# Kernel optimization log

Measured on AMD Instinct MI355X. Metric: run time of the kernel, lower is better.

## Reference

```python
import jax, jax.numpy as jnp
import numpy as np

B_SZ = 2
SEQ = 2048
D_MODEL = 2048
D_INNER = 4096
D_STATE = 128
D_CONV = 4
HEADDIM = 64
NHEADS = D_INNER // HEADDIM
CHUNK = 256
EPS = 1e-5


def segsum(a):
    # a: (..., T) -> (..., T, T) lower-triangular segment sums, -inf above diag
    T = a.shape[-1]
    cs = jnp.cumsum(a, axis=-1)
    ss = cs[..., :, None] - cs[..., None, :]
    mask = jnp.tril(jnp.ones((T, T), dtype=bool))
    return jnp.where(mask, ss, -jnp.inf)


def setup_inputs() -> dict:
    key = jax.random.key(0)
    ks = jax.random.split(key, 8)
    conv_dim = D_INNER + 2 * D_STATE
    d_in_proj = 2 * D_INNER + 2 * D_STATE + NHEADS
    x = jax.random.normal(ks[0], (B_SZ, SEQ, D_MODEL), jnp.float32)
    in_proj_w = jax.random.normal(ks[1], (d_in_proj, D_MODEL), jnp.float32) * 0.02
    conv_w = jax.random.normal(ks[2], (conv_dim, D_CONV), jnp.float32) * 0.2
    conv_b = jnp.zeros((conv_dim,), jnp.float32)
    dt0 = jax.random.uniform(ks[3], (NHEADS,), jnp.float32, 0.001, 0.1)
    dt_bias = jnp.log(jnp.expm1(dt0))  # inverse-softplus init as in mamba_ssm
    A_log = jnp.log(jax.random.uniform(ks[4], (NHEADS,), jnp.float32, 1.0, 16.0))
    D = jnp.ones((NHEADS,), jnp.float32)
    norm_w = jnp.ones((D_INNER,), jnp.float32)
    out_proj_w = jax.random.normal(ks[5], (D_MODEL, D_INNER), jnp.float32) * 0.02
    return {"x": x, "in_proj_w": in_proj_w, "conv_w": conv_w, "conv_b": conv_b,
            "dt_bias": dt_bias, "A_log": A_log, "D": D, "norm_w": norm_w,
            "out_proj_w": out_proj_w}


def reference(x, in_proj_w, conv_w, conv_b, dt_bias, A_log, D, norm_w, out_proj_w):
    b, L, _ = x.shape
    conv_dim = D_INNER + 2 * D_STATE
    # in_proj -> [z, xBC, dt]
    zxbcdt = jnp.einsum('bld,ed->ble', x, in_proj_w)
    z = zxbcdt[..., :D_INNER]
    xBC = zxbcdt[..., D_INNER:D_INNER + conv_dim]
    dt = jax.nn.softplus(zxbcdt[..., D_INNER + conv_dim:] + dt_bias)  # (b,L,H)
    # causal depthwise conv1d + silu
    xBC_t = jnp.transpose(xBC, (0, 2, 1))  # (b, conv_dim, L)
    conv_out = jax.lax.conv_general_dilated(
        xBC_t, conv_w[:, None, :], window_strides=(1,),
        padding=[(D_CONV - 1, 0)], feature_group_count=conv_dim)
    xBC = jax.nn.silu(jnp.transpose(conv_out + conv_b[:, None], (0, 2, 1)))
    x_ssm = xBC[..., :D_INNER].reshape(b, L, NHEADS, HEADDIM)
    Bm = xBC[..., D_INNER:D_INNER + D_STATE]          # (b,L,N) ngroups=1
    Cm = xBC[..., D_INNER + D_STATE:]                  # (b,L,N)
    A = -jnp.exp(A_log)                                # (H,)
    dA = dt * A                                        # (b,L,H)
    X = x_ssm * dt[..., None]                          # (b,L,H,P)
    # chunked SSD
    nc = L // CHUNK
    Xc = X.reshape(b, nc, CHUNK, NHEADS, HEADDIM)
    dAc = jnp.transpose(dA.reshape(b, nc, CHUNK, NHEADS), (0, 3, 1, 2))  # (b,h,c,l)
    Bc = Bm.reshape(b, nc, CHUNK, D_STATE)
    Cc = Cm.reshape(b, nc, CHUNK, D_STATE)
    Lmat = jnp.exp(segsum(dAc))                        # (b,h,c,l,l)
    Y_diag = jnp.einsum('bcln,bcsn,bhcls,bcshp->bclhp', Cc, Bc, Lmat, Xc)
    A_cs = jnp.cumsum(dAc, axis=-1)                    # (b,h,c,l)
    decay_states = jnp.exp(A_cs[..., -1:] - A_cs)
    states = jnp.einsum('bcln,bhcl,bclhp->bchpn', Bc, decay_states, Xc)
    chunk_sum = jnp.pad(A_cs[..., -1], ((0, 0), (0, 0), (1, 0)))  # (b,h,c+1)
    decay_chunk = jnp.exp(segsum(chunk_sum))           # (b,h,c+1,c+1)
    states_cat = jnp.concatenate([jnp.zeros_like(states[:, :1]), states], axis=1)
    prev = jnp.einsum('bhzc,bchpn->bzhpn', decay_chunk, states_cat)[:, :-1]
    Y_off = jnp.einsum('bcln,bchpn,bhcl->bclhp', Cc, prev, jnp.exp(A_cs))
    Y = (Y_diag + Y_off).reshape(b, L, NHEADS, HEADDIM)
    Y = Y + x_ssm * D[:, None]                          # skip connection per head
    y = Y.reshape(b, L, D_INNER)
    # gated RMSNorm: norm(y * silu(z)) * weight
    yg = y * jax.nn.silu(z)
    var = jnp.mean(yg * yg, axis=-1, keepdims=True)
    y = yg * jax.lax.rsqrt(var + EPS) * norm_w
    return jnp.einsum('ble,de->bld', y, out_proj_w)
```

## Files before the change

kernel.cpp:

```cpp
#include <hip/hip_runtime.h>
#include <math.h>

#define NBSZ 2
#define SEQ 2048
#define DMODEL 2048
#define DINNER 4096
#define DSTATE 128
#define NHEADS 64
#define CHUNK 256
#define NC 8
#define CONVDIM 4352
#define DINPROJ 8512

typedef unsigned short ushort_t;
typedef short short8 __attribute__((ext_vector_type(8)));
typedef float f32x4 __attribute__((ext_vector_type(4)));

__device__ __forceinline__ float bf2f(ushort_t u){
  union { float f; unsigned u; } x; x.u = ((unsigned)u) << 16; return x.f;
}
__device__ __forceinline__ ushort_t f2bf(float f){
  union { float f; unsigned u; } x; x.f = f;
  unsigned u = x.u;
  unsigned r = (u + 0x7fffu + ((u >> 16) & 1u)) >> 16;
  return (ushort_t)r;
}
__device__ __forceinline__ float exp_neg(float a){
  return expf(fminf(a, 0.f));
}
__device__ __forceinline__ void gload_lds16(const void* g, void* l) {
  __builtin_amdgcn_global_load_lds(
      (const __attribute__((address_space(1))) unsigned int*)g,
      (__attribute__((address_space(3))) unsigned int*)l, 16, 0, 0);
}

#define N_X   8388608LL
#define O_WIN 8388608LL
#define O_CW  25821184LL
#define O_CB  25838592LL
#define O_DTB 25842944LL
#define O_AL  25843008LL
#define O_DD  25843072LL
#define O_NW  25843136LL
#define O_WO  25847232LL
#define N_TOT 34235840LL
#define N_GRP (N_TOT / 8)

__global__ __launch_bounds__(256)
void convert_inputs(const void* __restrict__ x, const void* __restrict__ w_in,
                    const void* __restrict__ cw, const void* __restrict__ cb,
                    const void* __restrict__ dtb, const void* __restrict__ alog,
                    const void* __restrict__ dd, const void* __restrict__ nw,
                    const void* __restrict__ wout, ushort_t* __restrict__ dst) {
  bool bf = (((const unsigned*)dd)[0] == 0x3F803F80u);
  long long stride = (long long)gridDim.x * 256LL;
  for (long long g = (long long)blockIdx.x * 256 + threadIdx.x; g < N_GRP; g += stride) {
    long long i = g * 8;
    const void* src; long long off;
    if      (i < O_WIN) { src = x;    off = i; }
    else if (i < O_CW)  { src = w_in; off = i - O_WIN; }
    else if (i < O_CB)  { src = cw;   off = i - O_CW; }
    else if (i < O_DTB) { src = cb;   off = i - O_CB; }
    else if (i < O_AL)  { src = dtb;  off = i - O_DTB; }
    else if (i < O_DD)  { src = alog; off = i - O_AL; }
    else if (i < O_NW)  { src = dd;   off = i - O_DD; }
    else if (i < O_WO)  { src = nw;   off = i - O_NW; }
    else                { src = wout; off = i - O_WO; }
    if (bf) {
      *(int4*)(dst + i) = *(const int4*)((const ushort_t*)src + off);
    } else {
      float4 a = *(const float4*)((const float*)src + off);
      float4 b = *(const float4*)((const float*)src + off + 4);
      short8 o;
      o[0] = (short)f2bf(a.x); o[1] = (short)f2bf(a.y);
      o[2] = (short)f2bf(a.z); o[3] = (short)f2bf(a.w);
      o[4] = (short)f2bf(b.x); o[5] = (short)f2bf(b.y);
      o[6] = (short)f2bf(b.z); o[7] = (short)f2bf(b.w);
      *(short8*)(dst + i) = o;
    }
  }
}

__global__ __launch_bounds__(256)
void gemm_bt(const ushort_t* __restrict__ A, const ushort_t* __restrict__ B,
             ushort_t* __restrict__ C, int M, int N, int K) {
  __shared__ __align__(16) ushort_t sA[128][64];
  __shared__ __align__(16) ushort_t sB[128][64];
  int tid = threadIdx.x;
  int wave = tid >> 6, lane = tid & 63, quad = lane >> 4, l16 = lane & 15;
  int m0 = blockIdx.x * 128, n0 = blockIdx.y * 128;
  int wm = (wave >> 1) * 64, wn = (wave & 1) * 64;
  int rsub = lane >> 3, csub = lane & 7;
  int swc = ((csub ^ rsub) & 7) * 8;
  int srow = wave * 8 + rsub;
  f32x4 acc[4][4] = {};
  int r7 = l16 & 7;
  for (int k0 = 0; k0 < K; k0 += 64) {
    const ushort_t* Ag = A + (size_t)(m0 + srow) * K + k0 + swc;
#pragma unroll
    for (int i = 0; i < 4; ++i)
      gload_lds16(Ag + (size_t)(i * 32) * K, &sA[wave * 8 + i * 32][0]);
#pragma unroll
    for (int i = 0; i < 4; ++i) {
      int br = n0 + srow + i * 32;
      if (br > N - 1) br = N - 1;
      gload_lds16(B + (size_t)br * K + k0 + swc, &sB[wave * 8 + i * 32][0]);
    }
    __syncthreads();
#pragma unroll
    for (int kk = 0; kk < 64; kk += 32) {
      int g = (kk >> 3) + quad;
      int sw = ((g ^ r7) & 7) * 8;
      short8 af[4], bfr[4];
#pragma unroll
      for (int i = 0; i < 4; ++i) af[i]  = *(const short8*)&sA[wm + i*16 + l16][sw];
#pragma unroll
      for (int j = 0; j < 4; ++j) bfr[j] = *(const short8*)&sB[wn + j*16 + l16][sw];
#pragma unroll
      for (int i = 0; i < 4; ++i)
#pragma unroll
        for (int j = 0; j < 4; ++j)
          acc[i][j] = __builtin_amdgcn_mfma_f32_16x16x32_bf16(af[i], bfr[j], acc[i][j], 0, 0, 0);
    }
    __syncthreads();
  }
#pragma unroll
  for (int i = 0; i < 4; ++i) {
    int row = m0 + wm + i*16 + quad*4;
#pragma unroll
    for (int j = 0; j < 4; ++j) {
      int col = n0 + wn + j*16 + l16;
      if (col < N) {
#pragma unroll
        for (int r = 0; r < 4; ++r)
          C[(size_t)(row + r) * N + col] = f2bf(acc[i][j][r]);
      }
    }
  }
}

__global__ __launch_bounds__(256)
void gemm_bt_splitk(const ushort_t* __restrict__ A, const ushort_t* __restrict__ B,
                    ushort_t* __restrict__ Cpart, int M, int N, int Kstride, int Klen) {
  __shared__ __align__(16) ushort_t sA[128][64];
  __shared__ __align__(16) ushort_t sB[128][64];
  int tid = threadIdx.x;
  int wave = tid >> 6, lane = tid & 63, quad = lane >> 4, l16 = lane & 15;
  int m0 = blockIdx.x * 128, n0 = blockIdx.y * 128;
  int wm = (wave >> 1) * 64, wn = (wave & 1) * 64;
  int rsub = lane >> 3, csub = lane & 7;
  int swc = ((csub ^ rsub) & 7) * 8;
  int srow = wave * 8 + rsub;
  const ushort_t* Ab = A + (size_t)blockIdx.z * Klen;
  const ushort_t* Bb = B + (size_t)blockIdx.z * Klen;
  ushort_t* Cp = Cpart + (size_t)blockIdx.z * M * N;
  f32x4 acc[4][4] = {};
  int r7 = l16 & 7;
  for (int k0 = 0; k0 < Klen; k0 += 64) {
    const ushort_t* Ag = Ab + (size_t)(m0 + srow) * Kstride + k0 + swc;
    const ushort_t* Bg = Bb + (size_t)(n0 + srow) * Kstride + k0 + swc;
#pragma unroll
    for (int i = 0; i < 4; ++i)
      gload_lds16(Ag + (size_t)(i * 32) * Kstride, &sA[wave * 8 + i * 32][0]);
#pragma unroll
    for (int i = 0; i < 4; ++i)
      gload_lds16(Bg + (size_t)(i * 32) * Kstride, &sB[wave * 8 + i * 32][0]);
    __syncthreads();
#pragma unroll
    for (int kk = 0; kk < 64; kk += 32) {
      int g = (kk >> 3) + quad;
      int sw = ((g ^ r7) & 7) * 8;
      short8 af[4], bfr[4];
#pragma unroll
      for (int i = 0; i < 4; ++i) af[i]  = *(const short8*)&sA[wm + i*16 + l16][sw];
#pragma unroll
      for (int j = 0; j < 4; ++j) bfr[j] = *(const short8*)&sB[wn + j*16 + l16][sw];
#pragma unroll
      for (int i = 0; i < 4; ++i)
#pragma unroll
        for (int j = 0; j < 4; ++j)
          acc[i][j] = __builtin_amdgcn_mfma_f32_16x16x32_bf16(af[i], bfr[j], acc[i][j], 0, 0, 0);
    }
    __syncthreads();
  }
#pragma unroll
  for (int i = 0; i < 4; ++i) {
    int row = m0 + wm + i*16 + quad*4;
#pragma unroll
    for (int j = 0; j < 4; ++j) {
      int col = n0 + wn + j*16 + l16;
#pragma unroll
      for (int r = 0; r < 4; ++r)
        Cp[(size_t)(row + r) * N + col] = f2bf(acc[i][j][r]);
    }
  }
}

__global__ __launch_bounds__(256)
void reduce_out(const ushort_t* __restrict__ p0, const ushort_t* __restrict__ p1,
                void* __restrict__ out, const unsigned* __restrict__ probe) {
  long long i = ((long long)blockIdx.x * 256 + threadIdx.x) * 8;
  short8 a = *(const short8*)(p0 + i);
  short8 b = *(const short8*)(p1 + i);
  float v[8];
#pragma unroll
  for (int q = 0; q < 8; ++q) {
    v[q] = bf2f((ushort_t)a[q]) + bf2f((ushort_t)b[q]);
    if (!(fabsf(v[q]) < 1e30f)) v[q] = 12345.0f;
  }
  if (probe[0] == 0x3F800000u) {
    float* of = (float*)out + i;
    *(float4*)of     = {v[0], v[1], v[2], v[3]};
    *(float4*)(of+4) = {v[4], v[5], v[6], v[7]};
  } else {
    short8 s;
#pragma unroll
    for (int q = 0; q < 8; ++q) s[q] = (short)f2bf(v[q]);
    *(short8*)((ushort_t*)out + i) = s;
  }
}

__global__ __launch_bounds__(256)
void conv_silu(const ushort_t* __restrict__ zx, const ushort_t* __restrict__ cw,
               const ushort_t* __restrict__ cb, ushort_t* __restrict__ xbc) {
  int idx = blockIdx.x * 256 + threadIdx.x;
  int c8 = (idx % (CONVDIM / 8)) * 8;
  int l  = (idx / (CONVDIM / 8)) % SEQ;
  int b  = idx / ((CONVDIM / 8) * SEQ);
  float acc[8];
  short8 bias = *(const short8*)(cb + c8);
#pragma unroll
  for (int q = 0; q < 8; ++q) acc[q] = bf2f((ushort_t)bias[q]);
  short8 wv[4];
#pragma unroll
  for (int m = 0; m < 4; ++m) wv[m] = *(const short8*)(cw + c8 * 4 + m * 8);
#pragma unroll
  for (int k = 0; k < 4; ++k) {
    int ll = l - 3 + k;
    if (ll >= 0) {
      short8 xv = *(const short8*)(zx + ((size_t)b * SEQ + ll) * DINPROJ + DINNER + c8);
#pragma unroll
      for (int q = 0; q < 8; ++q) {
        int j = q * 4 + k;
        acc[q] += bf2f((ushort_t)xv[q]) * bf2f((ushort_t)wv[j >> 3][j & 7]);
      }
    }
  }
  short8 o;
#pragma unroll
  for (int q = 0; q < 8; ++q) {
    float sig = 1.f / (1.f + expf(-acc[q]));
    o[q] = (short)f2bf(acc[q] * sig);
  }
  *(short8*)(xbc + ((size_t)b * SEQ + l) * CONVDIM + c8) = o;
}

__global__ __launch_bounds__(256)
void transpose_B(const ushort_t* __restrict__ xbc, ushort_t* __restrict__ Bt) {
  __shared__ ushort_t tile[64][72];
  int bid = blockIdx.x;
  int ft = bid & 1;
  int st = (bid >> 1) & 31;
  int b  = bid >> 6;
  int t = threadIdx.x;
  int r = t >> 2, c0 = (t & 3) * 16;
  const ushort_t* src = xbc + ((size_t)b * SEQ + st * 64 + r) * CONVDIM + DINNER + ft * 64 + c0;
  *(int4*)&tile[r][c0]     = *(const int4*)src;
  *(int4*)&tile[r][c0 + 8] = *(const int4*)(src + 8);
  __syncthreads();
  int f = t >> 2, s0 = (t & 3) * 16;
  ushort_t tmp[16];
#pragma unroll
  for (int q = 0; q < 16; ++q) tmp[q] = tile[s0 + q][f];
  ushort_t* dst = Bt + ((size_t)b * 128 + ft * 64 + f) * SEQ + st * 64 + s0;
  *(int4*)dst       = *(int4*)&tmp[0];
  *(int4*)(dst + 8) = *(int4*)&tmp[8];
}

__global__ __launch_bounds__(256)
void chunk_cumsum(const ushort_t* __restrict__ zx, const ushort_t* __restrict__ dt_bias,
                  const ushort_t* __restrict__ A_log,
                  float* __restrict__ dt, float* __restrict__ cs) {
  int bid = blockIdx.x;
  int c = bid % NC, h = (bid / NC) % NHEADS, b = bid / (NC * NHEADS);
  int t = threadIdx.x;
  int l = c * CHUNK + t;
  float v = bf2f(zx[(size_t)(b * SEQ + l) * DINPROJ + DINNER + CONVDIM + h]) + bf2f(dt_bias[h]);
  float sp = (v > 20.f) ? v : log1pf(expf(v));
  dt[(size_t)(b * SEQ + l) * NHEADS + h] = sp;
  float A = -expf(bf2f(A_log[h]));
  __shared__ float sh[CHUNK];
  sh[t] = sp * A; __syncthreads();
  for (int off = 1; off < CHUNK; off <<= 1) {
    float add = (t >= off) ? sh[t - off] : 0.f;
    __syncthreads();
    sh[t] += add;
    __syncthreads();
  }
  cs[(size_t)bid * CHUNK + t] = sh[t];
}

__global__ __launch_bounds__(256)
void states_kernel(const ushort_t* __restrict__ xbc, const ushort_t* __restrict__ Bt,
                   const float* __restrict__ dt, const float* __restrict__ cs,
                   float* __restrict__ states) {
  int bid = blockIdx.x;
  int h = bid % NHEADS, c = (bid / NHEADS) % NC, b = bid / (NHEADS * NC);
  int tid = threadIdx.x, wave = tid >> 6, lane = tid & 63, quad = lane >> 4, l16 = lane & 15;
  __shared__ __align__(16) ushort_t sXt[64][264];
  int l0 = c * CHUNK;
  const float* csC = cs + ((size_t)((b * NHEADS + h) * NC + c)) * CHUNK;
  {
    int l = tid;
    float cl = csC[CHUNK - 1];
    float scale = dt[((size_t)b * SEQ + l0 + l) * NHEADS + h] * exp_neg(cl - csC[l]);
    const ushort_t* xrow = xbc + ((size_t)b * SEQ + l0 + l) * CONVDIM + h * 64;
#pragma unroll
    for (int pp = 0; pp < 64; pp += 8) {
      short8 v = *(const short8*)(xrow + pp);
#pragma unroll
      for (int q = 0; q < 8; ++q) sXt[pp + q][l] = f2bf(bf2f((ushort_t)v[q]) * scale);
    }
  }
  __syncthreads();
  f32x4 acc[4][2] = {};
  for (int ks = 0; ks < 8; ++ks) {
    int k0 = ks * 32;
    short8 bfr[2];
#pragma unroll
    for (int j = 0; j < 2; ++j) {
      int n = wave * 32 + j * 16 + l16;
      bfr[j] = *(const short8*)(Bt + ((size_t)b * 128 + n) * SEQ + l0 + k0 + quad * 8);
    }
#pragma unroll
    for (int i = 0; i < 4; ++i) {
      short8 af = *(const short8*)&sXt[i * 16 + l16][k0 + quad * 8];
#pragma unroll
      for (int j = 0; j < 2; ++j)
        acc[i][j] = __builtin_amdgcn_mfma_f32_16x16x32_bf16(af, bfr[j], acc[i][j], 0, 0, 0);
    }
  }
  float* sp = states + (size_t)bid * 64 * 128;
#pragma unroll
  for (int i = 0; i < 4; ++i) {
    int p = i * 16 + quad * 4;
#pragma unroll
    for (int j = 0; j < 2; ++j) {
      int n = wave * 32 + j * 16 + l16;
#pragma unroll
      for (int r = 0; r < 4; ++r) sp[(size_t)(p + r) * 128 + n] = acc[i][j][r];
    }
  }
}

__global__ __launch_bounds__(256)
void chunk_scan(const float* __restrict__ states, const float* __restrict__ cs,
                ushort_t* __restrict__ prev) {
  int bid = blockIdx.x;
  int half = bid & 1;
  int bh = bid >> 1;
  int h = bh % NHEADS, b = bh / NHEADS;
  int t = threadIdx.x;
  int base = half * 4096;
  float p_[16];
#pragma unroll
  for (int i = 0; i < 16; ++i) p_[i] = 0.f;
  for (int c = 0; c < NC; ++c) {
    size_t off = ((size_t)((b * NC + c) * NHEADS + h)) * 8192 + base;
    ushort_t* pv = prev + off;
#pragma unroll
    for (int i = 0; i < 16; ++i) pv[t + i * 256] = f2bf(p_[i]);
    float g = exp_neg(cs[((size_t)((b * NHEADS + h) * NC + c)) * CHUNK + CHUNK - 1]);
    const float* st = states + off;
#pragma unroll
    for (int i = 0; i < 16; ++i) p_[i] = p_[i] * g + st[t + i * 256];
  }
}

__global__ __launch_bounds__(256)
void ycombine_kernel(const ushort_t* __restrict__ xbc, const float* __restrict__ dt,
                     const float* __restrict__ cs, const ushort_t* __restrict__ prev,
                     const ushort_t* __restrict__ Dv, ushort_t* __restrict__ Y) {
  int bid = blockIdx.x;
  int h = bid % NHEADS, c = (bid / NHEADS) % NC, b = bid / (NHEADS * NC);
  int tid = threadIdx.x, wave = tid >> 6, lane = tid & 63, quad = lane >> 4, l16 = lane & 15;
  __shared__ __align__(16) ushort_t sXt[64][264];
  __shared__ __align__(16) ushort_t sP[4][64][40];
  __shared__ float sCs[CHUNK];
  int l0 = c * CHUNK;
  const float* csC = cs + ((size_t)((b * NHEADS + h) * NC + c)) * CHUNK;
  sCs[tid] = csC[tid];
  {
    int l = tid;
    float scale = dt[((size_t)b * SEQ + l0 + l) * NHEADS + h];
    const ushort_t* xrow = xbc + ((size_t)b * SEQ + l0 + l) * CONVDIM + h * 64;
#pragma unroll
    for (int pp = 0; pp < 64; pp += 8) {
      short8 v = *(const short8*)(xrow + pp);
#pragma unroll
      for (int q = 0; q < 8; ++q) sXt[pp + q][l] = f2bf(bf2f((ushort_t)v[q]) * scale);
    }
  }
  __syncthreads();
  f32x4 acc[4][4] = {};
  const ushort_t* prevH = prev + ((size_t)((b * NC + c) * NHEADS + h)) * 8192;
  for (int ks = 0; ks < 4; ++ks) {
    int k0 = ks * 32;
    short8 bfr[4];
#pragma unroll
    for (int j = 0; j < 4; ++j)
      bfr[j] = *(const short8*)(prevH + (size_t)(j * 16 + l16) * 128 + k0 + quad * 8);
#pragma unroll
    for (int i = 0; i < 4; ++i) {
      int lrow = (wave + 4 * i) * 16 + l16;
      const ushort_t* cp = xbc + ((size_t)b * SEQ + l0 + lrow) * CONVDIM + DINNER + DSTATE + k0 + quad * 8;
      short8 raw = *(const short8*)cp;
      float e = exp_neg(sCs[lrow]);
      short8 af;
#pragma unroll
      for (int jj = 0; jj < 8; ++jj) af[jj] = (short)f2bf(bf2f((ushort_t)raw[jj]) * e);
#pragma unroll
      for (int j = 0; j < 4; ++j)
        acc[i][j] = __builtin_amdgcn_mfma_f32_16x16x32_bf16(af, bfr[j], acc[i][j], 0, 0, 0);
    }
  }
  int nsb = (wave >= 2) ? 8 : 7;
  for (int sb = 0; sb < nsb; ++sb) {
    int s0 = sb * 32;
    f32x4 sacc[4][2] = {};
    for (int ks = 0; ks < 4; ++ks) {
      int k0 = ks * 32;
      short8 bfr[2];
#pragma unroll
      for (int j = 0; j < 2; ++j) {
        const ushort_t* bp = xbc + ((size_t)b * SEQ + l0 + s0 + j * 16 + l16) * CONVDIM + DINNER + k0 + quad * 8;
        bfr[j] = *(const short8*)bp;
      }
#pragma unroll
      for (int i = 0; i < 4; ++i) {
        int ti = wave + 4 * i;
        if (s0 <= ti * 16 + 15) {
          const ushort_t* cp2 = xbc + ((size_t)b * SEQ + l0 + ti * 16 + l16) * CONVDIM + DINNER + DSTATE + k0 + quad * 8;
          short8 af = *(const short8*)cp2;
#pragma unroll
          for (int j = 0; j < 2; ++j)
            sacc[i][j] = __builtin_amdgcn_mfma_f32_16x16x32_bf16(af, bfr[j], sacc[i][j], 0, 0, 0);
        }
      }
    }
#pragma unroll
    for (int i = 0; i < 4; ++i) {
      int ti = wave + 4 * i;
      if (s0 <= ti * 16 + 15) {
#pragma unroll
        for (int j = 0; j < 2; ++j) {
          int scol = s0 + j * 16 + l16;
          float cs_s = sCs[scol];
#pragma unroll
          for (int r = 0; r < 4; ++r) {
            int lrow = ti * 16 + quad * 4 + r;
            float L = (lrow >= scol) ? exp_neg(sCs[lrow] - cs_s) : 0.f;
            sP[wave][i * 16 + quad * 4 + r][j * 16 + l16] = f2bf(sacc[i][j][r] * L);
          }
        }
      }
    }
    asm volatile("s_waitcnt lgkmcnt(0)" ::: "memory");
    short8 bfx[4];
#pragma unroll
    for (int j = 0; j < 4; ++j)
      bfx[j] = *(const short8*)&sXt[j * 16 + l16][s0 + quad * 8];
#pragma unroll
    for (int i = 0; i < 4; ++i) {
      int ti = wave + 4 * i;
      if (s0 <= ti * 16 + 15) {
        short8 af = *(const short8*)&sP[wave][i * 16 + l16][quad * 8];
#pragma unroll
        for (int j = 0; j < 4; ++j)
          acc[i][j] = __builtin_amdgcn_mfma_f32_16x16x32_bf16(af, bfx[j], acc[i][j], 0, 0, 0);
      }
    }
  }
  float Dh = bf2f(Dv[h]);
#pragma unroll
  for (int i = 0; i < 4; ++i) {
    int ti = wave + 4 * i;
#pragma unroll
    for (int r = 0; r < 4; ++r) {
      int lrow = ti * 16 + quad * 4 + r;
      const ushort_t* xrow = xbc + ((size_t)b * SEQ + l0 + lrow) * CONVDIM + h * 64;
      ushort_t* yrow = Y + ((size_t)b * SEQ + l0 + lrow) * DINNER + h * 64;
#pragma unroll
      for (int j = 0; j < 4; ++j) {
        int p = j * 16 + l16;
        yrow[p] = f2bf(acc[i][j][r] + Dh * bf2f(xrow[p]));
      }
    }
  }
}

__global__ __launch_bounds__(256)
void gate_norm(const ushort_t* __restrict__ Y, const ushort_t* __restrict__ zx,
               const ushort_t* __restrict__ nw, ushort_t* __restrict__ out) {
  int bl = blockIdx.x, t = threadIdx.x;
  int wave = t >> 6, lane = t & 63;
  const ushort_t* yrow = Y + (size_t)bl * DINNER + t * 16;
  const ushort_t* zrow = zx + (size_t)bl * DINPROJ + t * 16;
  float vals[16];
  float ss = 0.f;
#pragma unroll
  for (int i = 0; i < 16; i += 8) {
    short8 yv = *(const short8*)(yrow + i);
    short8 zv = *(const short8*)(zrow + i);
#pragma unroll
    for (int q = 0; q < 8; ++q) {
      float y = bf2f((ushort_t)yv[q]);
      float z = bf2f((ushort_t)zv[q]);
      float sig = 1.f / (1.f + expf(-z));
      float g = y * z * sig;
      vals[i + q] = g;
      ss += g * g;
    }
  }
#pragma unroll
  for (int off = 32; off > 0; off >>= 1) ss += __shfl_down(ss, off);
  __shared__ float red[4];
  if (lane == 0) red[wave] = ss;
  __syncthreads();
  float inv = rsqrtf((red[0] + red[1] + red[2] + red[3]) / (float)DINNER + 1e-5f);
  ushort_t* orow = out + (size_t)bl * DINNER + t * 16;
  const ushort_t* wrow = nw + t * 16;
#pragma unroll
  for (int i = 0; i < 16; ++i)
    orow[i] = f2bf(vals[i] * inv * bf2f(wrow[i]));
}

extern "C" void kernel_launch(void* const* d_in, const int* in_sizes, int n_in,
                              void* d_out, int out_size, void* d_ws, size_t ws_size,
                              hipStream_t stream) {
  char* p = (char*)d_ws;
  ushort_t* cvt = (ushort_t*)p; p += (size_t)N_TOT * 2;
  const ushort_t* x       = cvt;
  const ushort_t* w_in    = cvt + O_WIN;
  const ushort_t* conv_w  = cvt + O_CW;
  const ushort_t* conv_b  = cvt + O_CB;
  const ushort_t* dt_bias = cvt + O_DTB;
  const ushort_t* A_log   = cvt + O_AL;
  const ushort_t* Dv      = cvt + O_DD;
  const ushort_t* norm_w  = cvt + O_NW;
  const ushort_t* w_out   = cvt + O_WO;

  ushort_t* zx    = (ushort_t*)p; p += (size_t)NBSZ * SEQ * DINPROJ * 2;
  ushort_t* xbc   = (ushort_t*)p; p += (size_t)NBSZ * SEQ * CONVDIM * 2;
  float*    dt    = (float*)p;    p += (size_t)NBSZ * SEQ * NHEADS * 4;
  float*    cs    = (float*)p;    p += (size_t)NBSZ * NHEADS * NC * CHUNK * 4;
  ushort_t* Bt    = (ushort_t*)p; p += (size_t)NBSZ * 128 * SEQ * 2;
  ushort_t* ynorm = (ushort_t*)p; p += (size_t)NBSZ * SEQ * DINNER * 2;
  float*    states = (float*)cvt;
  ushort_t* prev   = (ushort_t*)((char*)cvt + (size_t)NBSZ * NC * NHEADS * 8192 * 4);
  ushort_t* Y = (ushort_t*)states;
  ushort_t* parts  = zx;

  int M = NBSZ * SEQ;
  convert_inputs<<<4096, 256, 0, stream>>>(d_in[0], d_in[1], d_in[2], d_in[3],
                                           d_in[4], d_in[5], d_in[6], d_in[7],
                                           d_in[8], cvt);
  gemm_bt<<<dim3(M / 128, (DINPROJ + 127) / 128), 256, 0, stream>>>(x, w_in, zx, M, DINPROJ, DMODEL);
  conv_silu<<<NBSZ * SEQ * (CONVDIM / 8) / 256, 256, 0, stream>>>(zx, conv_w, conv_b, xbc);
  transpose_B<<<NBSZ * 32 * 2, 256, 0, stream>>>(xbc, Bt);
  chunk_cumsum<<<NBSZ * NHEADS * NC, 256, 0, stream>>>(zx, dt_bias, A_log, dt, cs);
  states_kernel<<<NBSZ * NC * NHEADS, 256, 0, stream>>>(xbc, Bt, dt, cs, states);
  chunk_scan<<<NBSZ * NHEADS * 2, 256, 0, stream>>>(states, cs, prev);
  ycombine_kernel<<<NBSZ * NC * NHEADS, 256, 0, stream>>>(xbc, dt, cs, prev, Dv, Y);
  gate_norm<<<M, 256, 0, stream>>>(Y, zx, norm_w, ynorm);
  gemm_bt_splitk<<<dim3(M / 128, DMODEL / 128, 2), 256, 0, stream>>>(ynorm, w_out, parts,
                                                                     M, DMODEL, DINNER, DINNER / 2);
  reduce_out<<<(M * DMODEL) / 2048, 256, 0, stream>>>(parts, parts + (size_t)M * DMODEL,
                                                      d_out, (const unsigned*)d_in[6]);
}
```

Measured before the change: 645.9 us.

## Split in_proj GEMM launch, use wave-shuffle cumsum, store chunk states in bf16

```diff
diff --git a/kernel.cpp b/kernel.cpp
--- a/kernel.cpp
+++ b/kernel.cpp
@@ -83,12 +83,12 @@
 
 __global__ __launch_bounds__(256)
 void gemm_bt(const ushort_t* __restrict__ A, const ushort_t* __restrict__ B,
-             ushort_t* __restrict__ C, int M, int N, int K) {
+             ushort_t* __restrict__ C, int M, int N, int K, int nb) {
   __shared__ __align__(16) ushort_t sA[128][64];
   __shared__ __align__(16) ushort_t sB[128][64];
   int tid = threadIdx.x;
   int wave = tid >> 6, lane = tid & 63, quad = lane >> 4, l16 = lane & 15;
-  int m0 = blockIdx.x * 128, n0 = blockIdx.y * 128;
+  int m0 = blockIdx.x * 128, n0 = nb + blockIdx.y * 128;
   int wm = (wave >> 1) * 64, wn = (wave & 1) * 64;
   int rsub = lane >> 3, csub = lane & 7;
   int swc = ((csub ^ rsub) & 7) * 8;
@@ -283,27 +283,31 @@
                   float* __restrict__ dt, float* __restrict__ cs) {
   int bid = blockIdx.x;
   int c = bid % NC, h = (bid / NC) % NHEADS, b = bid / (NC * NHEADS);
-  int t = threadIdx.x;
+  int t = threadIdx.x, wave = t >> 6, lane = t & 63;
   int l = c * CHUNK + t;
   float v = bf2f(zx[(size_t)(b * SEQ + l) * DINPROJ + DINNER + CONVDIM + h]) + bf2f(dt_bias[h]);
   float sp = (v > 20.f) ? v : log1pf(expf(v));
   dt[(size_t)(b * SEQ + l) * NHEADS + h] = sp;
   float A = -expf(bf2f(A_log[h]));
-  __shared__ float sh[CHUNK];
-  sh[t] = sp * A; __syncthreads();
-  for (int off = 1; off < CHUNK; off <<= 1) {
-    float add = (t >= off) ? sh[t - off] : 0.f;
-    __syncthreads();
-    sh[t] += add;
-    __syncthreads();
-  }
-  cs[(size_t)bid * CHUNK + t] = sh[t];
+  float x = sp * A;
+#pragma unroll
+  for (int off = 1; off < 64; off <<= 1) {
+    float y = __shfl_up(x, off);
+    if (lane >= off) x += y;
+  }
+  __shared__ float wsum[4];
+  if (lane == 63) wsum[wave] = x;
+  __syncthreads();
+  float base = 0.f;
+#pragma unroll
+  for (int w = 0; w < 3; ++w) if (w < wave) base += wsum[w];
+  cs[(size_t)bid * CHUNK + t] = x + base;
 }
 
 __global__ __launch_bounds__(256)
 void states_kernel(const ushort_t* __restrict__ xbc, const ushort_t* __restrict__ Bt,
                    const float* __restrict__ dt, const float* __restrict__ cs,
-                   float* __restrict__ states) {
+                   ushort_t* __restrict__ states) {
   int bid = blockIdx.x;
   int h = bid % NHEADS, c = (bid / NHEADS) % NC, b = bid / (NHEADS * NC);
   int tid = threadIdx.x, wave = tid >> 6, lane = tid & 63, quad = lane >> 4, l16 = lane & 15;
@@ -340,7 +344,7 @@
         acc[i][j] = __builtin_amdgcn_mfma_f32_16x16x32_bf16(af, bfr[j], acc[i][j], 0, 0, 0);
     }
   }
-  float* sp = states + (size_t)bid * 64 * 128;
+  ushort_t* sp = states + (size_t)bid * 64 * 128;
 #pragma unroll
   for (int i = 0; i < 4; ++i) {
     int p = i * 16 + quad * 4;
@@ -348,13 +352,13 @@
     for (int j = 0; j < 2; ++j) {
       int n = wave * 32 + j * 16 + l16;
 #pragma unroll
-      for (int r = 0; r < 4; ++r) sp[(size_t)(p + r) * 128 + n] = acc[i][j][r];
-    }
-  }
-}
-
-__global__ __launch_bounds__(256)
-void chunk_scan(const float* __restrict__ states, const float* __restrict__ cs,
+      for (int r = 0; r < 4; ++r) sp[(size_t)(p + r) * 128 + n] = f2bf(acc[i][j][r]);
+    }
+  }
+}
+
+__global__ __launch_bounds__(256)
+void chunk_scan(const ushort_t* __restrict__ states, const float* __restrict__ cs,
                 ushort_t* __restrict__ prev) {
   int bid = blockIdx.x;
   int half = bid & 1;
@@ -371,9 +375,9 @@
 #pragma unroll
     for (int i = 0; i < 16; ++i) pv[t + i * 256] = f2bf(p_[i]);
     float g = exp_neg(cs[((size_t)((b * NHEADS + h) * NC + c)) * CHUNK + CHUNK - 1]);
-    const float* st = states + off;
-#pragma unroll
-    for (int i = 0; i < 16; ++i) p_[i] = p_[i] * g + st[t + i * 256];
+    const ushort_t* st = states + off;
+#pragma unroll
+    for (int i = 0; i < 16; ++i) p_[i] = p_[i] * g + bf2f(st[t + i * 256]);
   }
 }
 
@@ -556,16 +560,17 @@
   float*    cs    = (float*)p;    p += (size_t)NBSZ * NHEADS * NC * CHUNK * 4;
   ushort_t* Bt    = (ushort_t*)p; p += (size_t)NBSZ * 128 * SEQ * 2;
   ushort_t* ynorm = (ushort_t*)p; p += (size_t)NBSZ * SEQ * DINNER * 2;
-  float*    states = (float*)cvt;
+  ushort_t* states = cvt;
   ushort_t* prev   = (ushort_t*)((char*)cvt + (size_t)NBSZ * NC * NHEADS * 8192 * 4);
-  ushort_t* Y = (ushort_t*)states;
+  ushort_t* Y = cvt;
   ushort_t* parts  = zx;
 
   int M = NBSZ * SEQ;
   convert_inputs<<<4096, 256, 0, stream>>>(d_in[0], d_in[1], d_in[2], d_in[3],
                                            d_in[4], d_in[5], d_in[6], d_in[7],
                                            d_in[8], cvt);
-  gemm_bt<<<dim3(M / 128, (DINPROJ + 127) / 128), 256, 0, stream>>>(x, w_in, zx, M, DINPROJ, DMODEL);
+  gemm_bt<<<dim3(M / 128, 34), 256, 0, stream>>>(x, w_in, zx, M, DINPROJ, DMODEL, 0);
+  gemm_bt<<<dim3(M / 128, 33), 256, 0, stream>>>(x, w_in, zx, M, DINPROJ, DMODEL, 4352);
   conv_silu<<<NBSZ * SEQ * (CONVDIM / 8) / 256, 256, 0, stream>>>(zx, conv_w, conv_b, xbc);
   transpose_B<<<NBSZ * 32 * 2, 256, 0, stream>>>(xbc, Bt);
   chunk_cumsum<<<NBSZ * NHEADS * NC, 256, 0, stream>>>(zx, dt_bias, A_log, dt, cs);
```

After: 654.5 us. Within noise of the previous version (+1.3%).
